# Performance work log

Measured on AMD Instinct MI355X. Metric: run time of the kernel, lower is better.

Reference implementation:

```python
import jax, jax.numpy as jnp
import numpy as np

B, C, H, W = 4, 64, 128, 128
KH = KW = 3
K = KH * KW          # 9 neighbours
E = 64               # offset-cnn embedding channels
CK = C * K           # 576
MAX_DIST = 8.0
GROUPS = 1           # NonlocalBlock groups arg


def _conv(x, w, b=None, padding=0, groups=1):
    out = jax.lax.conv_general_dilated(
        x, w, (1, 1), [(padding, padding), (padding, padding)],
        dimension_numbers=('NCHW', 'OIHW', 'NCHW'), feature_group_count=groups)
    return out if b is None else out + b[None, :, None, None]


def _convnext(x, dw, pw1, pw2):
    y = _conv(x, dw, padding=3, groups=x.shape[1])
    y = _conv(jax.nn.relu(_conv(y, pw1)), pw2)
    return x + y


def _offset_cnn(x, ws, bs):
    y = jax.nn.leaky_relu(_conv(x, ws[0], bs[0]), 0.1)
    for i in range(1, 5):
        y = jax.nn.leaky_relu(_conv(y, ws[i], bs[i], padding=1), 0.1)
    return _conv(y, ws[5], bs[5])


def _deform_neighbourhood(x, offsets):
    # x: (B,C,H,W); offsets: (B, 2*K, H, W) as (k, [dy,dx]) pairs.
    b, c, h, w = x.shape
    off = offsets.reshape(b, K, 2, h, w)
    dy, dx = off[:, :, 0], off[:, :, 1]                       # (B,K,H,W)
    base = jnp.stack(jnp.meshgrid(jnp.arange(KH) - KH // 2,
                                  jnp.arange(KW) - KW // 2,
                                  indexing='ij'), 0).reshape(2, K).astype(x.dtype)
    hh = jnp.arange(h, dtype=x.dtype)[None, None, :, None]
    ww = jnp.arange(w, dtype=x.dtype)[None, None, None, :]
    py = hh + base[0][None, :, None, None] + dy               # (B,K,H,W)
    px = ww + base[1][None, :, None, None] + dx

    y0 = jnp.floor(py); x0 = jnp.floor(px)
    wy1 = py - y0; wy0 = 1.0 - wy1
    wx1 = px - x0; wx0 = 1.0 - wx1
    xf = x.reshape(b, c, h * w)

    def gather(yy, xx):
        valid = (yy >= 0) & (yy < h) & (xx >= 0) & (xx < w)
        yc = jnp.clip(yy, 0, h - 1).astype(jnp.int32)
        xc = jnp.clip(xx, 0, w - 1).astype(jnp.int32)
        idx = (yc * w + xc).reshape(b, -1)                    # (B, K*H*W)
        vals = jax.vmap(lambda m, i: m[:, i])(xf, idx)        # (B,C,K*H*W)
        return vals.reshape(b, c, K, h, w) * valid[:, None].astype(x.dtype)

    out = (gather(y0, x0) * (wy0 * wx0)[:, None]
           + gather(y0, x0 + 1) * (wy0 * wx1)[:, None]
           + gather(y0 + 1, x0) * (wy1 * wx0)[:, None]
           + gather(y0 + 1, x0 + 1) * (wy1 * wx1)[:, None])
    return out.reshape(b, c * K, h, w)                        # layout (feature, neighbour)


def _forward(x, enc_dw, enc_pw1, enc_pw2, dec_dw, dec_pw1, dec_pw2,
             off_w1, off_b1, off_w2, off_b2, off_w3, off_b3,
             off_w4, off_b4, off_w5, off_b5, off_w6, off_b6,
             dct_w, wie_w1, wie_w2, wie_w3, wie_w4, wie_w5, wie_w6,
             inv_w1, inv_w2):
    x = _convnext(x, enc_dw, enc_pw1, enc_pw2)
    offsets = MAX_DIST * jnp.tanh(_offset_cnn(
        x, [off_w1, off_w2, off_w3, off_w4, off_w5, off_w6],
        [off_b1, off_b2, off_b3, off_b4, off_b5, off_b6]))
    xb = _deform_neighbourhood(x, offsets)                    # (B, C*K, H, W)
    dct = _conv(xb, dct_w, groups=C // GROUPS)                # per-feature neighbour mixing
    y = _conv(xb, wie_w1)
    y = jax.nn.relu(_conv(y, wie_w2, padding=1, groups=CK))
    y = _conv(y, wie_w3)
    y = jax.nn.relu(_conv(y, wie_w4, padding=1, groups=CK))
    y = _conv(y, wie_w5)
    wiener = jax.nn.sigmoid(_conv(y, wie_w6, padding=1, groups=CK))
    out = _conv(_conv(wiener * dct, inv_w1, groups=C // GROUPS), inv_w2)
    return _convnext(out, dec_dw, dec_pw1, dec_pw2)


def setup_inputs() -> dict:
    key = jax.random.key(0)
    ks = iter(jax.random.split(key, 40))

    def w(shape, scale=None):
        fan_in = int(np.prod(shape[1:]))
        s = (1.0 / np.sqrt(fan_in)) if scale is None else scale
        return jax.random.normal(next(ks), shape, jnp.float32) * s

    inp = {
        'x': jax.random.normal(next(ks), (B, C, H, W), jnp.float32),
        'enc_dw': w((C, 1, 7, 7)), 'enc_pw1': w((2 * C, C, 1, 1)), 'enc_pw2': w((C, 2 * C, 1, 1)),
        'dec_dw': w((C, 1, 7, 7)), 'dec_pw1': w((2 * C, C, 1, 1)), 'dec_pw2': w((C, 2 * C, 1, 1)),
        'off_w1': w((E, C, 1, 1)), 'off_b1': w((E,), 0.01),
        'off_w2': w((E, E, 3, 3)), 'off_b2': w((E,), 0.01),
        'off_w3': w((E, E, 3, 3)), 'off_b3': w((E,), 0.01),
        'off_w4': w((E, E, 3, 3)), 'off_b4': w((E,), 0.01),
        'off_w5': w((E, E, 3, 3)), 'off_b5': w((E,), 0.01),
        'off_w6': w((2 * K, E, 1, 1), 0.02), 'off_b6': w((2 * K,), 0.01),
        'dct_w': w((CK, K, 1, 1)),
        'wie_w1': w((CK, CK, 1, 1)), 'wie_w2': w((CK, 1, 3, 3)),
        'wie_w3': w((CK, CK, 1, 1)), 'wie_w4': w((CK, 1, 3, 3)),
        'wie_w5': w((CK, CK, 1, 1)), 'wie_w6': w((CK, 1, 3, 3)),
        'inv_w1': w((CK, K, 1, 1)), 'inv_w2': w((C, CK, 1, 1)),
    }
    return inp


def reference(x, enc_dw, enc_pw1, enc_pw2, dec_dw, dec_pw1, dec_pw2,
              off_w1, off_b1, off_w2, off_b2, off_w3, off_b3,
              off_w4, off_b4, off_w5, off_b5, off_w6, off_b6,
              dct_w, wie_w1, wie_w2, wie_w3, wie_w4, wie_w5, wie_w6,
              inv_w1, inv_w2):
    return _forward(x, enc_dw, enc_pw1, enc_pw2, dec_dw, dec_pw1, dec_pw2,
                    off_w1, off_b1, off_w2, off_b2, off_w3, off_b3,
                    off_w4, off_b4, off_w5, off_b5, off_w6, off_b6,
                    dct_w, wie_w1, wie_w2, wie_w3, wie_w4, wie_w5, wie_w6,
                    inv_w1, inv_w2)
```

## Files before the change

kernel.cpp:

```cpp
#include <hip/hip_runtime.h>
#include <math.h>

#define HWp 16384
#define Wp 128
#define Hp 128
#define Bp 4
#define Cp 64
#define CKp 576

typedef unsigned int u32;
typedef unsigned short ushortt;
typedef __attribute__((ext_vector_type(8))) short short8;
typedef __attribute__((ext_vector_type(4))) float float4v;

__device__ __forceinline__ ushortt f2b(float f) {
  union { float f; u32 u; } x; x.f = f;
  u32 r = x.u + 0x7fff + ((x.u >> 16) & 1);
  return (ushortt)(r >> 16);
}
__device__ __forceinline__ float b2f(ushortt h) {
  union { u32 u; float f; } x; x.u = ((u32)h) << 16; return x.f;
}
__device__ __forceinline__ float blo(u32 t) {
  union { u32 u; float f; } x; x.u = t << 16; return x.f;
}
__device__ __forceinline__ float bhi(u32 t) {
  union { u32 u; float f; } x; x.u = t & 0xffff0000u; return x.f;
}
__device__ __forceinline__ void gll(const ushortt* g, ushortt* l) {
  __builtin_amdgcn_global_load_lds(
      (const __attribute__((address_space(1))) u32*)g,
      (__attribute__((address_space(3))) u32*)l, 16, 0, 0);
}

__global__ __launch_bounds__(256)
void dwconv7_lds(const float* __restrict__ in, const float* __restrict__ w,
                 ushortt* __restrict__ out) {
  int bc = blockIdx.y;
  int tid = threadIdx.x;
  int y0 = blockIdx.x * 2;
  __shared__ float ws[49];
  __shared__ float tile[8][136];
  if (tid < 49) ws[tid] = w[(bc & 63) * 49 + tid];
  if (tid < 48) {
    int r = tid / 6, cc = tid % 6;
    tile[r][cc < 3 ? cc : 128 + cc] = 0.f;
  }
  const float* ip = in + (size_t)bc * HWp;
  #pragma unroll
  for (int i = 0; i < 4; i++) {
    int idx = tid + 256 * i;
    int r = idx >> 7, xx = idx & 127;
    int yy = y0 - 3 + r;
    tile[r][xx + 3] = (yy >= 0 && yy < Hp) ? ip[yy * Wp + xx] : 0.f;
  }
  __syncthreads();
  int ty = tid >> 7, x = tid & 127;
  float acc = 0.f;
  #pragma unroll
  for (int dy = 0; dy < 7; dy++)
    #pragma unroll
    for (int dx = 0; dx < 7; dx++)
      acc += tile[ty + dy][x + dx] * ws[dy * 7 + dx];
  out[(size_t)bc * HWp + (y0 + ty) * Wp + x] = f2b(acc);
}

template<int CIN, int ACT, int MODE>
__global__ __launch_bounds__(256)
void pw_bf(const ushortt* __restrict__ in, const ushortt* __restrict__ wt,
           const float* __restrict__ resid, void* __restrict__ outv, int Cout) {
  int tid = threadIdx.x;
  int wid = tid >> 6, lane = tid & 63;
  int q = lane >> 4, m = lane & 15;
  int px0 = blockIdx.x * 128, co0 = blockIdx.y * 64;
  int pxh = (wid & 1) * 64, coh = (wid >> 1) * 32;
  float4v acc[4][2];
  #pragma unroll
  for (int i = 0; i < 4; i++)
    #pragma unroll
    for (int j = 0; j < 2; j++) acc[i][j] = (float4v){0.f, 0.f, 0.f, 0.f};

  #pragma unroll
  for (int k0 = 0; k0 < CIN; k0 += 32) {
    short8 a[4], b[2];
    #pragma unroll
    for (int j = 0; j < 2; j++)
      b[j] = *(const short8*)&wt[(size_t)(co0 + coh + j * 16 + m) * CIN + k0 + q * 8];
    #pragma unroll
    for (int i = 0; i < 4; i++)
      a[i] = *(const short8*)&in[(size_t)(px0 + pxh + i * 16 + m) * CIN + k0 + q * 8];
    #pragma unroll
    for (int i = 0; i < 4; i++)
      #pragma unroll
      for (int j = 0; j < 2; j++)
        acc[i][j] = __builtin_amdgcn_mfma_f32_16x16x32_bf16(a[i], b[j], acc[i][j], 0, 0, 0);
  }

  #pragma unroll
  for (int j = 0; j < 2; j++) {
    int co = co0 + coh + j * 16 + m;
    #pragma unroll
    for (int i = 0; i < 4; i++) {
      int pxb = px0 + pxh + i * 16 + q * 4;
      int bl = pxb >> 14, pim = pxb & 16383;
      if (MODE == 0) {
        #pragma unroll
        for (int r = 0; r < 4; r++) {
          float v = acc[i][j][r];
          if (ACT == 1) v = fmaxf(v, 0.f);
          ((ushortt*)outv)[(size_t)(pxb + r) * Cout + co] = f2b(v);
        }
      } else {
        float4 rr = *(const float4*)&resid[(size_t)(bl * 64 + co) * HWp + pim];
        float v0 = acc[i][j][0] + rr.x, v1 = acc[i][j][1] + rr.y;
        float v2 = acc[i][j][2] + rr.z, v3 = acc[i][j][3] + rr.w;
        if (MODE == 1) {
          ushortt* ob = (ushortt*)outv;
          ob[(size_t)(pxb + 0) * 64 + co] = f2b(v0);
          ob[(size_t)(pxb + 1) * 64 + co] = f2b(v1);
          ob[(size_t)(pxb + 2) * 64 + co] = f2b(v2);
          ob[(size_t)(pxb + 3) * 64 + co] = f2b(v3);
        } else {
          float4 w4; w4.x = v0; w4.y = v1; w4.z = v2; w4.w = v3;
          *(float4*)&((float*)outv)[(size_t)(bl * 64 + co) * HWp + pim] = w4;
        }
      }
    }
  }
}

template<int TAPS>
__global__ __launch_bounds__(256)
void conv_bf(const ushortt* __restrict__ in, const ushortt* __restrict__ wt,
             const float* __restrict__ bias, ushortt* __restrict__ out) {
  int tid = threadIdx.x;
  int wid = tid >> 6, lane = tid & 63;
  int q = lane >> 4, m = lane & 15;
  int bx = blockIdx.x, b = blockIdx.y;
  int y = bx >> 1;
  int c0 = ((bx & 1) << 6) + ((wid & 1) << 5);
  int coW = (wid >> 1) << 5;
  size_t ibase = (size_t)b * HWp;

  float4v acc[2][2];
  #pragma unroll
  for (int i = 0; i < 2; i++)
    #pragma unroll
    for (int j = 0; j < 2; j++) acc[i][j] = (float4v){0.f, 0.f, 0.f, 0.f};
  short8 zz = {0, 0, 0, 0, 0, 0, 0, 0};

  #pragma unroll
  for (int k = 0; k < TAPS; k++) {
    int dy = (TAPS == 9) ? (k / 3 - 1) : 0;
    int dx = (TAPS == 9) ? (k % 3 - 1) : 0;
    int yy = y + dy;
    if (TAPS == 9 && (yy < 0 || yy >= Hp)) continue;
    #pragma unroll
    for (int ch = 0; ch < 2; ch++) {
      int ci0 = ch * 32 + q * 8;
      short8 bfr[2], afr[2];
      #pragma unroll
      for (int j = 0; j < 2; j++)
        bfr[j] = *(const short8*)&wt[(size_t)(k * 64 + coW + j * 16 + m) * 64 + ci0];
      #pragma unroll
      for (int i = 0; i < 2; i++) {
        int col = c0 + i * 16 + m + dx;
        bool vld = (TAPS == 1) || ((unsigned)col < (unsigned)Wp);
        int colc = min(max(col, 0), Wp - 1);
        short8 h = *(const short8*)&in[(ibase + (size_t)yy * Wp + colc) * 64 + ci0];
        afr[i] = vld ? h : zz;
      }
      #pragma unroll
      for (int i = 0; i < 2; i++)
        #pragma unroll
        for (int j = 0; j < 2; j++)
          acc[i][j] = __builtin_amdgcn_mfma_f32_16x16x32_bf16(afr[i], bfr[j], acc[i][j], 0, 0, 0);
    }
  }

  #pragma unroll
  for (int j = 0; j < 2; j++) {
    int co = coW + j * 16 + m;
    float bv = bias[co];
    #pragma unroll
    for (int i = 0; i < 2; i++) {
      #pragma unroll
      for (int r = 0; r < 4; r++) {
        size_t px = ibase + (size_t)y * Wp + c0 + i * 16 + q * 4 + r;
        float v = acc[i][j][r] + bv;
        v = v > 0.f ? v : 0.1f * v;
        out[px * 64 + co] = f2b(v);
      }
    }
  }
}

__global__ __launch_bounds__(256)
void t64b(const ushortt* __restrict__ in, ushortt* __restrict__ out) {
  __shared__ ushortt tl[64 * 65];
  int tid = threadIdx.x;
  int b = blockIdx.y;
  int px0 = blockIdx.x * 64;
  int lpx = tid & 63, c4 = tid >> 6;
  const ushortt* ip = in + (size_t)b * 64 * HWp;
  #pragma unroll
  for (int i = 0; i < 16; i++) {
    int c = c4 + 4 * i;
    tl[lpx * 65 + c] = ip[(size_t)c * HWp + px0 + lpx];
  }
  __syncthreads();
  int ci = tid & 63, pr = tid >> 6;
  #pragma unroll
  for (int i = 0; i < 16; i++) {
    int r = pr + 4 * i;
    out[((size_t)b * HWp + px0 + r) * 64 + ci] = tl[r * 65 + ci];
  }
}

__global__ __launch_bounds__(256)
void repack_all(const float* __restrict__ w1a, const float* __restrict__ w3a,
                const float* __restrict__ w5a, const float* __restrict__ inv2,
                const float* __restrict__ d2, const float* __restrict__ d4,
                const float* __restrict__ d6, const float* __restrict__ ow1,
                const float* __restrict__ ow2, const float* __restrict__ ow3,
                const float* __restrict__ ow4, const float* __restrict__ ow5,
                const float* __restrict__ p1, const float* __restrict__ p2,
                const float* __restrict__ p3, const float* __restrict__ p4,
                ushortt* __restrict__ wb, ushortt* __restrict__ wbi2,
                ushortt* __restrict__ wdwb, ushortt* __restrict__ wc1,
                ushortt* __restrict__ wc2, ushortt* __restrict__ wpw) {
  int b = blockIdx.x;
  int tid = threadIdx.x;
  if (b < 4320) {
    int which = b / 1440;
    int idx = (b - which * 1440) * 256 + tid;
    const float* in = which == 0 ? w1a : which == 1 ? w3a : w5a;
    int cop = idx / 576, cip = idx % 576;
    ushortt v = 0;
    if (cop < 576) {
      int co = (cop & 63) * 9 + (cop >> 6);
      int ci = (cip & 63) * 9 + (cip >> 6);
      v = f2b(in[(size_t)co * 576 + ci]);
    }
    wb[(size_t)which * 640 * 576 + idx] = v;
  } else if (b < 4464) {
    int idx = (b - 4320) * 256 + tid;
    if (idx < 64 * 576) {
      int co = idx / 576, cip = idx % 576;
      int ci = (cip & 63) * 9 + (cip >> 6);
      wbi2[idx] = f2b(inv2[(size_t)co * 576 + ci]);
    }
  } else if (b < 4525) {
    int idx = (b - 4464) * 256 + tid;
    if (idx < 3 * 5184) {
      int which = idx / 5184, r = idx % 5184;
      const float* in = which == 0 ? d2 : which == 1 ? d4 : d6;
      int tap = r / 576, chp = r % 576;
      int ch = (chp & 63) * 9 + (chp >> 6);
      wdwb[idx] = f2b(in[ch * 9 + tap]);
    }
  } else if (b < 4541) {
    int idx = (b - 4525) * 256 + tid;
    if (idx < 4096) wc1[idx] = f2b(ow1[idx]);
  } else if (b < 5117) {
    int bb = b - 4541;
    int which = bb / 144;
    int idx = (bb - which * 144) * 256 + tid;
    if (idx < 36864) {
      const float* in = which == 0 ? ow2 : which == 1 ? ow3 : which == 2 ? ow4 : ow5;
      int k = idx >> 12, r = idx & 4095;
      int co = r >> 6, ci = r & 63;
      wc2[which * 36864 + idx] = f2b(in[(size_t)(co * 64 + ci) * 9 + k]);
    }
  } else {
    int bb = b - 5117;
    int which = bb / 32;
    int idx = (bb - which * 32) * 256 + tid;
    if (idx < 8192) {
      const float* in = which == 0 ? p1 : which == 1 ? p2 : which == 2 ? p3 : p4;
      wpw[which * 8192 + idx] = f2b(in[idx]);
    }
  }
}

__global__ __launch_bounds__(256)
void off6_nhwc(const ushortt* __restrict__ hi, const float* __restrict__ wgt,
               const float* __restrict__ bias, float* __restrict__ out) {
  __shared__ float Wl[18 * 64];
  for (int i = threadIdx.x; i < 18 * 64; i += 256) Wl[i] = wgt[i];
  __syncthreads();
  int px = blockIdx.x * 256 + threadIdx.x;
  int b = px >> 14, pim = px & 16383;
  float acc[18];
  #pragma unroll
  for (int j = 0; j < 18; j++) acc[j] = 0.f;
  const uint4* ph = (const uint4*)(hi + (size_t)px * 64);
  for (int g = 0; g < 8; g++) {
    uint4 H = ph[g];
    u32 hw[4] = {H.x, H.y, H.z, H.w};
    #pragma unroll
    for (int t = 0; t < 4; t++) {
      float v0 = blo(hw[t]);
      float v1 = bhi(hw[t]);
      int ci = g * 8 + t * 2;
      #pragma unroll
      for (int j = 0; j < 18; j++)
        acc[j] += Wl[j * 64 + ci] * v0 + Wl[j * 64 + ci + 1] * v1;
    }
  }
  #pragma unroll
  for (int j = 0; j < 18; j++)
    out[((size_t)b * 18 + j) * HWp + pim] = 8.f * tanhf(acc[j] + bias[j]);
}

__global__ __launch_bounds__(256)
void deform_x(const ushortt* __restrict__ xn0, const float* __restrict__ offs0,
              ushortt* __restrict__ xb) {
  int lin = blockIdx.x;
  int xcd = lin & 7, local = lin >> 3;
  int rowi = local >> 4, bx = local & 15;
  int tid = threadIdx.x;
  int wid = tid >> 6, lane = tid & 63;
  int c2 = lane & 31, ps = lane >> 5;
  int pg = (xcd * 32 + rowi) * 128 + bx * 8 + wid * 2 + ps;
  int bl = pg >> 14, p = pg & 16383;
  const ushortt* xn = xn0 + (size_t)bl * HWp * 64;
  const float* offs = offs0 + (size_t)bl * 18 * HWp;
  int yi = p >> 7, xi = p & 127;
  #pragma unroll
  for (int k = 0; k < 9; k++) {
    float dy = offs[(size_t)(2 * k) * HWp + p];
    float dx = offs[(size_t)(2 * k + 1) * HWp + p];
    float py = (float)yi + (float)(k / 3 - 1) + dy;
    float px = (float)xi + (float)(k % 3 - 1) + dx;
    float y0f = floorf(py), x0f = floorf(px);
    float wy1 = py - y0f, wy0 = 1.f - wy1;
    float wx1 = px - x0f, wx0 = 1.f - wx1;
    int y0 = (int)y0f, x0 = (int)x0f;
    bool vy0 = (y0 >= 0 && y0 < Hp), vy1 = (y0 + 1 >= 0 && y0 + 1 < Hp);
    bool vx0 = (x0 >= 0 && x0 < Wp), vx1 = (x0 + 1 >= 0 && x0 + 1 < Wp);
    int yc0 = min(max(y0, 0), Hp - 1), yc1 = min(max(y0 + 1, 0), Hp - 1);
    int xc0 = min(max(x0, 0), Wp - 1), xc1 = min(max(x0 + 1, 0), Wp - 1);
    float w00 = wy0 * wx0 * ((vy0 && vx0) ? 1.f : 0.f);
    float w01 = wy0 * wx1 * ((vy0 && vx1) ? 1.f : 0.f);
    float w10 = wy1 * wx0 * ((vy1 && vx0) ? 1.f : 0.f);
    float w11 = wy1 * wx1 * ((vy1 && vx1) ? 1.f : 0.f);
    u32 t00 = *(const u32*)&xn[(size_t)(yc0 * Wp + xc0) * 64 + c2 * 2];
    u32 t01 = *(const u32*)&xn[(size_t)(yc0 * Wp + xc1) * 64 + c2 * 2];
    u32 t10 = *(const u32*)&xn[(size_t)(yc1 * Wp + xc0) * 64 + c2 * 2];
    u32 t11 = *(const u32*)&xn[(size_t)(yc1 * Wp + xc1) * 64 + c2 * 2];
    float a = blo(t00) * w00 + blo(t01) * w01 + blo(t10) * w10 + blo(t11) * w11;
    float bv = bhi(t00) * w00 + bhi(t01) * w01 + bhi(t10) * w10 + bhi(t11) * w11;
    u32 pk = (u32)f2b(a) | (((u32)f2b(bv)) << 16);
    *(u32*)&xb[(size_t)pg * 576 + 64 * k + c2 * 2] = pk;
  }
}

__global__ __launch_bounds__(256)
void gemm128(const ushortt* __restrict__ X, const ushortt* __restrict__ Wb,
             ushortt* __restrict__ out) {
  __shared__ ushortt Xs[128 * 32];
  __shared__ ushortt Wsh[128 * 32];
  int tid = threadIdx.x;
  int lin = blockIdx.x + blockIdx.y * 5;
  int xcd = lin & 7, loc = lin >> 3;
  int co_t = loc % 5;
  int px_t = xcd * 32 + loc / 5;
  int co0 = co_t * 128, px0 = px_t * 128;
  int r0 = tid >> 2;
  int sch = (tid & 3) ^ ((tid >> 3) & 3);
  size_t gx0 = (size_t)(px0 + r0) * 576 + sch * 8;
  size_t gx1 = gx0 + (size_t)64 * 576;
  size_t gw0 = (size_t)(co0 + r0) * 576 + sch * 8;
  size_t gw1 = gw0 + (size_t)64 * 576;
  int wid = tid >> 6, lane = tid & 63;
  int q = lane >> 4, m = lane & 15;
  int qx = (q ^ ((m >> 1) & 3)) * 8;
  int pxh = (wid & 1) * 64, coh = (wid >> 1) * 64;
  float4v acc[4][4];
  #pragma unroll
  for (int i = 0; i < 4; i++)
    #pragma unroll
    for (int j = 0; j < 4; j++) acc[i][j] = (float4v){0.f, 0.f, 0.f, 0.f};

  for (int k0 = 0; k0 < 576; k0 += 32) {
    __syncthreads();
    gll(X + gx0 + k0,  &Xs[tid * 8]);
    gll(X + gx1 + k0,  &Xs[2048 + tid * 8]);
    gll(Wb + gw0 + k0, &Wsh[tid * 8]);
    gll(Wb + gw1 + k0, &Wsh[2048 + tid * 8]);
    __syncthreads();
    short8 a[4], b[4];
    #pragma unroll
    for (int i = 0; i < 4; i++)
      a[i] = *(const short8*)&Xs[(pxh + i * 16 + m) * 32 + qx];
    #pragma unroll
    for (int j = 0; j < 4; j++)
      b[j] = *(const short8*)&Wsh[(coh + j * 16 + m) * 32 + qx];
    #pragma unroll
    for (int i = 0; i < 4; i++)
      #pragma unroll
      for (int j = 0; j < 4; j++)
        acc[i][j] = __builtin_amdgcn_mfma_f32_16x16x32_bf16(a[i], b[j], acc[i][j], 0, 0, 0);
  }

  #pragma unroll
  for (int j = 0; j < 4; j++) {
    int co = co0 + coh + j * 16 + m;
    if (co >= 576) continue;
    #pragma unroll
    for (int i = 0; i < 4; i++) {
      int pxb = px0 + pxh + i * 16 + q * 4;
      #pragma unroll
      for (int r = 0; r < 4; r++)
        out[(size_t)(pxb + r) * 576 + co] = f2b(acc[i][j][r]);
    }
  }
}

__global__ __launch_bounds__(256)
void gemm64o2(const ushortt* __restrict__ X, const ushortt* __restrict__ Wb,
              float* __restrict__ outv) {
  __shared__ ushortt Xs[128 * 32];
  __shared__ ushortt Wsh[64 * 32];
  int tid = threadIdx.x;
  int lin = blockIdx.x;
  int xcd = lin & 7, local = lin >> 3;
  int px0 = (xcd * 32 + local) * 128;
  int srow = tid >> 2;
  int sch = (tid & 3) ^ ((tid >> 3) & 3);
  size_t gxo0 = (size_t)(px0 + srow) * 576 + sch * 8;
  size_t gxo1 = gxo0 + (size_t)64 * 576;
  size_t gwo  = (size_t)srow * 576 + sch * 8;
  int wid = tid >> 6, lane = tid & 63;
  int q = lane >> 4, m = lane & 15;
  int qx = (q ^ ((m >> 1) & 3)) * 8;
  int pxh = (wid & 1) * 64, coh = (wid >> 1) * 32;
  float4v acc[4][2];
  #pragma unroll
  for (int i = 0; i < 4; i++)
    #pragma unroll
    for (int j = 0; j < 2; j++) acc[i][j] = (float4v){0.f, 0.f, 0.f, 0.f};

  for (int k0 = 0; k0 < 576; k0 += 32) {
    __syncthreads();
    gll(X + gxo0 + k0,  &Xs[tid * 8]);
    gll(X + gxo1 + k0,  &Xs[2048 + tid * 8]);
    gll(Wb + gwo + k0,  &Wsh[tid * 8]);
    __syncthreads();
    short8 a[4], b[2];
    #pragma unroll
    for (int i = 0; i < 4; i++)
      a[i] = *(const short8*)&Xs[(pxh + i * 16 + m) * 32 + qx];
    #pragma unroll
    for (int j = 0; j < 2; j++)
      b[j] = *(const short8*)&Wsh[(coh + j * 16 + m) * 32 + qx];
    #pragma unroll
    for (int i = 0; i < 4; i++)
      #pragma unroll
      for (int j = 0; j < 2; j++)
        acc[i][j] = __builtin_amdgcn_mfma_f32_16x16x32_bf16(a[i], b[j], acc[i][j], 0, 0, 0);
  }

  #pragma unroll
  for (int j = 0; j < 2; j++) {
    int co = coh + j * 16 + m;
    #pragma unroll
    for (int i = 0; i < 4; i++) {
      int pxb = px0 + pxh + i * 16 + q * 4;
      int bl = pxb >> 14, pim = pxb & 16383;
      float4 r;
      r.x = acc[i][j][0]; r.y = acc[i][j][1];
      r.z = acc[i][j][2]; r.w = acc[i][j][3];
      *(float4*)&outv[(size_t)(bl * 64 + co) * HWp + pim] = r;
    }
  }
}

template<int ACT>
__global__ __launch_bounds__(256)
void dw3x3_v3(const ushortt* __restrict__ in, const ushortt* __restrict__ wt,
              ushortt* __restrict__ out) {
  int lin = blockIdx.x;
  int xcd = lin & 7, local = lin >> 3;
  int g = local / 43, bxq = local - g * 43;
  int rg = xcd * 8 + g;
  int bz = rg >> 5, by = rg & 31;
  int tid = threadIdx.x;
  int pxl = tid / 72;
  int gg = tid - pxl * 72;
  if (pxl >= 3) return;
  int x = bxq * 3 + pxl;
  if (x >= Wp) return;
  int y0 = by * 4;
  size_t bbase = (size_t)bz * HWp;

  float w[9][8];
  #pragma unroll
  for (int t = 0; t < 9; t++) {
    uint4 wv = *(const uint4*)&wt[t * 576 + gg * 8];
    u32 wsw[4] = {wv.x, wv.y, wv.z, wv.w};
    #pragma unroll
    for (int p = 0; p < 4; p++) {
      w[t][2 * p]     = blo(wsw[p]);
      w[t][2 * p + 1] = bhi(wsw[p]);
    }
  }
  float acc[4][8];
  #pragma unroll
  for (int o = 0; o < 4; o++)
    #pragma unroll
    for (int c = 0; c < 8; c++) acc[o][c] = 0.f;

  #pragma unroll
  for (int ri = 0; ri < 6; ri++) {
    int yy = y0 - 1 + ri;
    bool vr = (yy >= 0 && yy < Hp);
    float v[3][8];
    #pragma unroll
    for (int dx = 0; dx < 3; dx++) {
      int xx = x + dx - 1;
      uint4 t4 = {0, 0, 0, 0};
      if (vr && xx >= 0 && xx < Wp)
        t4 = *(const uint4*)&in[(bbase + (size_t)yy * Wp + xx) * 576 + gg * 8];
      u32 tw[4] = {t4.x, t4.y, t4.z, t4.w};
      #pragma unroll
      for (int p = 0; p < 4; p++) {
        v[dx][2 * p]     = blo(tw[p]);
        v[dx][2 * p + 1] = bhi(tw[p]);
      }
    }
    #pragma unroll
    for (int o = 0; o < 4; o++) {
      int dy = ri - o;
      if (dy < 0 || dy > 2) continue;
      #pragma unroll
      for (int dx = 0; dx < 3; dx++)
        #pragma unroll
        for (int c = 0; c < 8; c++)
          acc[o][c] += w[dy * 3 + dx][c] * v[dx][c];
    }
  }

  #pragma unroll
  for (int o = 0; o < 4; o++) {
    int yy = y0 + o;
    u32 pk[4];
    #pragma unroll
    for (int p = 0; p < 4; p++) {
      float r0 = acc[o][2 * p], r1 = acc[o][2 * p + 1];
      if (ACT == 1) { r0 = fmaxf(r0, 0.f); r1 = fmaxf(r1, 0.f); }
      else { r0 = 1.f / (1.f + __expf(-r0)); r1 = 1.f / (1.f + __expf(-r1)); }
      pk[p] = (u32)f2b(r0) | (((u32)f2b(r1)) << 16);
    }
    uint4 o4; o4.x = pk[0]; o4.y = pk[1]; o4.z = pk[2]; o4.w = pk[3];
    *(uint4*)&out[(bbase + (size_t)yy * Wp + x) * 576 + gg * 8] = o4;
  }
}

__global__ __launch_bounds__(256)
void g9inv2(const ushortt* __restrict__ wien, const ushortt* __restrict__ xb,
            const float* __restrict__ wdct, const float* __restrict__ winv,
            ushortt* __restrict__ outb) {
  __shared__ float Wd[5184];
  __shared__ float Wi[5184];
  for (int i = threadIdx.x; i < 5184; i += 256) {
    Wd[i] = wdct[i];
    Wi[i] = winv[i];
  }
  __syncthreads();
  int lin = blockIdx.x;
  int xcd = lin & 7, local = lin >> 3;
  int rowi = local >> 5, bx = local & 31;
  size_t px = (size_t)((xcd * 32 + rowi) * 128 + bx * 4) + (threadIdx.x >> 6);
  int c = threadIdx.x & 63;
  float xr[9], v[9];
  #pragma unroll
  for (int t = 0; t < 9; t++) xr[t] = b2f(xb[px * 576 + 64 * t + c]);
  const float* wd = &Wd[c * 81];
  const float* wi = &Wi[c * 81];
  #pragma unroll
  for (int o = 0; o < 9; o++) {
    float d = 0.f;
    #pragma unroll
    for (int t = 0; t < 9; t++) d += wd[o * 9 + t] * xr[t];
    v[o] = b2f(wien[px * 576 + 64 * o + c]) * d;
  }
  #pragma unroll
  for (int j = 0; j < 9; j++) {
    float a = 0.f;
    #pragma unroll
    for (int o = 0; o < 9; o++) a += wi[j * 9 + o] * v[o];
    outb[px * 576 + 64 * j + c] = f2b(a);
  }
}

extern "C" void kernel_launch(void* const* d_in, const int* in_sizes, int n_in,
                              void* d_out, int out_size, void* d_ws, size_t ws_size,
                              hipStream_t stream) {
  const float* x       = (const float*)d_in[0];
  const float* enc_dw  = (const float*)d_in[1];
  const float* enc_pw1 = (const float*)d_in[2];
  const float* enc_pw2 = (const float*)d_in[3];
  const float* dec_dw  = (const float*)d_in[4];
  const float* dec_pw1 = (const float*)d_in[5];
  const float* dec_pw2 = (const float*)d_in[6];
  const float* off_w1  = (const float*)d_in[7];
  const float* off_b1  = (const float*)d_in[8];
  const float* off_w2  = (const float*)d_in[9];
  const float* off_b2  = (const float*)d_in[10];
  const float* off_w3  = (const float*)d_in[11];
  const float* off_b3  = (const float*)d_in[12];
  const float* off_w4  = (const float*)d_in[13];
  const float* off_b4  = (const float*)d_in[14];
  const float* off_w5  = (const float*)d_in[15];
  const float* off_b5  = (const float*)d_in[16];
  const float* off_w6  = (const float*)d_in[17];
  const float* off_b6  = (const float*)d_in[18];
  const float* dct_w   = (const float*)d_in[19];
  const float* wie_w1  = (const float*)d_in[20];
  const float* wie_w2  = (const float*)d_in[21];
  const float* wie_w3  = (const float*)d_in[22];
  const float* wie_w4  = (const float*)d_in[23];
  const float* wie_w5  = (const float*)d_in[24];
  const float* wie_w6  = (const float*)d_in[25];
  const float* inv_w1  = (const float*)d_in[26];
  const float* inv_w2  = (const float*)d_in[27];
  float* outp = (float*)d_out;

  const size_t NP = (size_t)Bp * HWp;
  const size_t REQ_FLOATS = NP * 64 + NP * 64 + NP * 128 +
                            2 * (size_t)HWp * CKp + (size_t)HWp * CKp;
  if (ws_size < REQ_FLOATS * sizeof(float)) return;

  float* ws  = (float*)d_ws;
  float* x1  = ws;
  float* t0  = x1 + NP * 64;
  float* t1  = t0 + NP * 64;
  float* bigA = t1 + NP * 128;
  float* bigB = bigA + (size_t)HWp * CKp;
  float* bigC = bigB + (size_t)HWp * CKp;
  ushortt* R1 = (ushortt*)bigA;
  ushortt* R2 = (ushortt*)bigB;
  ushortt* R3 = (ushortt*)bigC;
  ushortt* e1 = (ushortt*)bigA;

  float* wreg = t0 + NP * 18;
  ushortt* wb  = (ushortt*)wreg;
  ushortt* wbi2 = wb + 3 * 640 * 576;
  ushortt* wdwb = wbi2 + 64 * 576;
  ushortt* wc1  = wdwb + 3 * 5184;
  ushortt* wc2  = wc1 + 4096;
  ushortt* wpw  = wc2 + 4 * 36864;

  ushortt* xnAll = (ushortt*)t1;
  ushortt* oA = xnAll + NP * 64;
  ushortt* oB = oA + NP * 64;

  float* offs = t0;
  float* mid  = x1;

  dim3 blk(256);

  dwconv7_lds<<<dim3(Hp / 2, Bp * Cp), blk, 0, stream>>>(x, enc_dw, (ushortt*)t0);
  t64b<<<dim3(HWp / 64, Bp), blk, 0, stream>>>((const ushortt*)t0, oA);

  repack_all<<<dim3(5245), blk, 0, stream>>>(
      wie_w1, wie_w3, wie_w5, inv_w2, wie_w2, wie_w4, wie_w6, off_w1,
      off_w2, off_w3, off_w4, off_w5, enc_pw1, enc_pw2, dec_pw1, dec_pw2,
      wb, wbi2, wdwb, wc1, wc2, wpw);

  pw_bf<64, 1, 0><<<dim3(NP / 128, 2), blk, 0, stream>>>(oA, wpw, nullptr, e1, 128);
  pw_bf<128, 0, 1><<<dim3(NP / 128, 1), blk, 0, stream>>>(e1, wpw + 8192, x, xnAll, 64);

  conv_bf<1><<<dim3(HWp / 64, Bp), blk, 0, stream>>>(xnAll, wc1, off_b1, oA);
  conv_bf<9><<<dim3(HWp / 64, Bp), blk, 0, stream>>>(oA, wc2,             off_b2, oB);
  conv_bf<9><<<dim3(HWp / 64, Bp), blk, 0, stream>>>(oB, wc2 + 36864,     off_b3, oA);
  conv_bf<9><<<dim3(HWp / 64, Bp), blk, 0, stream>>>(oA, wc2 + 2 * 36864, off_b4, oB);
  conv_bf<9><<<dim3(HWp / 64, Bp), blk, 0, stream>>>(oB, wc2 + 3 * 36864, off_b5, oA);
  off6_nhwc<<<dim3(NP / 256), blk, 0, stream>>>(oA, off_w6, off_b6, offs);

  for (int bp = 0; bp < 2; bp++) {
    const ushortt* xn0 = xnAll + (size_t)(2 * bp) * HWp * 64;
    const float* off0 = offs + (size_t)(2 * bp) * 18 * HWp;
    float* mid0 = mid + (size_t)(2 * bp) * 64 * HWp;

    deform_x<<<dim3(4096), blk, 0, stream>>>(xn0, off0, R2);
    gemm128<<<dim3(5, 256), blk, 0, stream>>>(R2, wb, R3);
    dw3x3_v3<1><<<dim3(2752), blk, 0, stream>>>(R3, wdwb, R1);
    gemm128<<<dim3(5, 256), blk, 0, stream>>>(R1, wb + 640 * 576, R3);
    dw3x3_v3<1><<<dim3(2752), blk, 0, stream>>>(R3, wdwb + 5184, R1);
    gemm128<<<dim3(5, 256), blk, 0, stream>>>(R1, wb + 2 * 640 * 576, R3);
    dw3x3_v3<2><<<dim3(2752), blk, 0, stream>>>(R3, wdwb + 2 * 5184, R1);
    g9inv2<<<dim3(8192), blk, 0, stream>>>(R1, R2, dct_w, inv_w1, R3);
    gemm64o2<<<dim3(256), blk, 0, stream>>>(R3, wbi2, mid0);
  }

  dwconv7_lds<<<dim3(Hp / 2, Bp * Cp), blk, 0, stream>>>(mid, dec_dw, (ushortt*)bigB);
  t64b<<<dim3(HWp / 64, Bp), blk, 0, stream>>>((const ushortt*)bigB, oA);
  pw_bf<64, 1, 0><<<dim3(NP / 128, 2), blk, 0, stream>>>(oA, wpw + 2 * 8192, nullptr, e1, 128);
  pw_bf<128, 0, 2><<<dim3(NP / 128, 1), blk, 0, stream>>>(e1, wpw + 3 * 8192, mid, outp, 64);
}
```

Before: 896.5 us.

## Double-buffer LDS tiles in gemm128 and vectorize transposed output stores

Adds a two-stage LDS ping-pong in gemm128 so global-to-LDS loads for the next K slice are issued before the MFMAs on the current slice, replacing two barriers per iteration with one. The MFMA operand order is swapped so each lane holds four consecutive output channels, which lets the epilogue pack them into one 8-byte store instead of four scattered 2-byte stores. LDS usage doubles, which may lower occupancy, and the single barrier relies on the async loads having completed before the next read.

```diff
diff --git a/kernel.cpp b/kernel.cpp
--- a/kernel.cpp
+++ b/kernel.cpp
@@ -359,8 +359,8 @@
 __global__ __launch_bounds__(256)
 void gemm128(const ushortt* __restrict__ X, const ushortt* __restrict__ Wb,
              ushortt* __restrict__ out) {
-  __shared__ ushortt Xs[128 * 32];
-  __shared__ ushortt Wsh[128 * 32];
+  __shared__ ushortt Xs[2][4096];
+  __shared__ ushortt Wsh[2][4096];
   int tid = threadIdx.x;
   int lin = blockIdx.x + blockIdx.y * 5;
   int xcd = lin & 7, loc = lin >> 3;
@@ -383,37 +383,47 @@
     #pragma unroll
     for (int j = 0; j < 4; j++) acc[i][j] = (float4v){0.f, 0.f, 0.f, 0.f};
 
+  gll(X + gx0,  &Xs[0][tid * 8]);
+  gll(X + gx1,  &Xs[0][2048 + tid * 8]);
+  gll(Wb + gw0, &Wsh[0][tid * 8]);
+  gll(Wb + gw1, &Wsh[0][2048 + tid * 8]);
+  __syncthreads();
+
+  int cur = 0;
   for (int k0 = 0; k0 < 576; k0 += 32) {
+    if (k0 + 32 < 576) {
+      gll(X + gx0 + k0 + 32,  &Xs[cur ^ 1][tid * 8]);
+      gll(X + gx1 + k0 + 32,  &Xs[cur ^ 1][2048 + tid * 8]);
+      gll(Wb + gw0 + k0 + 32, &Wsh[cur ^ 1][tid * 8]);
+      gll(Wb + gw1 + k0 + 32, &Wsh[cur ^ 1][2048 + tid * 8]);
+    }
+    short8 a[4], b[4];
+    #pragma unroll
+    for (int i = 0; i < 4; i++)
+      a[i] = *(const short8*)&Xs[cur][(pxh + i * 16 + m) * 32 + qx];
+    #pragma unroll
+    for (int j = 0; j < 4; j++)
+      b[j] = *(const short8*)&Wsh[cur][(coh + j * 16 + m) * 32 + qx];
+    #pragma unroll
+    for (int i = 0; i < 4; i++)
+      #pragma unroll
+      for (int j = 0; j < 4; j++)
+        acc[i][j] = __builtin_amdgcn_mfma_f32_16x16x32_bf16(b[j], a[i], acc[i][j], 0, 0, 0);
     __syncthreads();
-    gll(X + gx0 + k0,  &Xs[tid * 8]);
-    gll(X + gx1 + k0,  &Xs[2048 + tid * 8]);
-    gll(Wb + gw0 + k0, &Wsh[tid * 8]);
-    gll(Wb + gw1 + k0, &Wsh[2048 + tid * 8]);
-    __syncthreads();
-    short8 a[4], b[4];
-    #pragma unroll
-    for (int i = 0; i < 4; i++)
-      a[i] = *(const short8*)&Xs[(pxh + i * 16 + m) * 32 + qx];
-    #pragma unroll
-    for (int j = 0; j < 4; j++)
-      b[j] = *(const short8*)&Wsh[(coh + j * 16 + m) * 32 + qx];
-    #pragma unroll
-    for (int i = 0; i < 4; i++)
-      #pragma unroll
-      for (int j = 0; j < 4; j++)
-        acc[i][j] = __builtin_amdgcn_mfma_f32_16x16x32_bf16(a[i], b[j], acc[i][j], 0, 0, 0);
+    cur ^= 1;
   }
 
   #pragma unroll
   for (int j = 0; j < 4; j++) {
-    int co = co0 + coh + j * 16 + m;
-    if (co >= 576) continue;
+    int cob = co0 + coh + j * 16 + q * 4;
+    if (cob >= 576) continue;
     #pragma unroll
     for (int i = 0; i < 4; i++) {
-      int pxb = px0 + pxh + i * 16 + q * 4;
-      #pragma unroll
-      for (int r = 0; r < 4; r++)
-        out[(size_t)(pxb + r) * 576 + co] = f2b(acc[i][j][r]);
+      size_t px = (size_t)(px0 + pxh + i * 16 + m);
+      u32 lo = (u32)f2b(acc[i][j][0]) | (((u32)f2b(acc[i][j][1])) << 16);
+      u32 hi = (u32)f2b(acc[i][j][2]) | (((u32)f2b(acc[i][j][3])) << 16);
+      uint2 st; st.x = lo; st.y = hi;
+      *(uint2*)&out[px * 576 + cob] = st;
     }
   }
 }
```

New measurement: 908.7 us. No clear change (+1.4%).
